# Kernel optimization log

Measured on AMD Instinct MI355X. Metric: run time of the kernel, lower is better.

The kernel has to match this reference:

```python
import jax, jax.numpy as jnp
import numpy as np

HIDDEN = 1024
HEADS = 16
HEAD_DIM = HIDDEN // HEADS

def setup_inputs() -> dict:
    key = jax.random.key(0)
    ks = jax.random.split(key, 11)
    B, T, D = 2, 2048, HIDDEN
    s = 1.0 / np.sqrt(D)
    return {
        "query": jax.random.normal(ks[0], (B, T, D), jnp.float32),
        "key": jax.random.normal(ks[1], (B, T, D), jnp.float32),
        "value": jax.random.normal(ks[2], (B, T, D), jnp.float32),
        "Wq": jax.random.normal(ks[3], (D, D), jnp.float32) * s,
        "bq": jnp.zeros((D,), jnp.float32),
        "Wk": jax.random.normal(ks[4], (D, D), jnp.float32) * s,
        "bk": jnp.zeros((D,), jnp.float32),
        "Wv": jax.random.normal(ks[5], (D, D), jnp.float32) * s,
        "bv": jnp.zeros((D,), jnp.float32),
        "Wo": jax.random.normal(ks[6], (D, D), jnp.float32) * s,
        "bo": jnp.zeros((D,), jnp.float32),
    }

def reference(query, key, value, Wq, bq, Wk, bk, Wv, bv, Wo, bo):
    B, Tq, D = query.shape
    Tk = key.shape[1]
    H, Hd = HEADS, HEAD_DIM
    # projections -> [B, H, T, Hd]
    Q = (query @ Wq + bq).reshape(B, Tq, H, Hd).transpose(0, 2, 1, 3)
    K = (key @ Wk + bk).reshape(B, Tk, H, Hd).transpose(0, 2, 1, 3)
    V = (value @ Wv + bv).reshape(B, Tk, H, Hd).transpose(0, 2, 1, 3)
    scale = jnp.sqrt(jnp.asarray(Hd, Q.dtype))
    scores = jnp.einsum('bhqd,bhkd->bhqk', Q, K) / scale  # [B,H,Tq,Tk]
    causal = jnp.triu(jnp.ones((Tq, Tk), bool), k=1)
    scores = jnp.where(causal[None, None], jnp.asarray(-jnp.inf, scores.dtype), scores)
    attn = jax.nn.softmax(scores, axis=-1)
    out = jnp.einsum('bhqk,bhkd->bhqd', attn, V)  # [B,H,Tq,Hd]
    out = out.transpose(0, 2, 1, 3).reshape(B, Tq, D)
    return out @ Wo + bo
```

## Files before the change

kernel.cpp:

```cpp
#include <hip/hip_runtime.h>
#include <hip/hip_bf16.h>


typedef __bf16 bf16_t;
typedef __bf16 bf16x4 __attribute__((ext_vector_type(4)));
typedef __bf16 bf16x8 __attribute__((ext_vector_type(8)));
typedef float f32x4 __attribute__((ext_vector_type(4)));
typedef float f32x16 __attribute__((ext_vector_type(16)));
typedef unsigned int u32;
typedef unsigned int u32x2v __attribute__((ext_vector_type(2)));
typedef unsigned int u32x4v __attribute__((ext_vector_type(4)));

#define D_MODEL 1024
#define SEQ_T   2048
#define NHEAD   16
#define HDIM    64
#define M_ROWS  4096
#define MEGA    (1024 * 1024)

__device__ __forceinline__ void gl2lds16(const void* g, void* l) {
    __builtin_amdgcn_global_load_lds((const __attribute__((address_space(1))) u32*)g,
                                     (__attribute__((address_space(3))) u32*)l, 16, 0, 0);
}

__device__ __forceinline__ u32 pk2(float a, float b) {
    unsigned short x = __builtin_bit_cast(unsigned short, (bf16_t)a);
    unsigned short y = __builtin_bit_cast(unsigned short, (bf16_t)b);
    return (u32)x | ((u32)y << 16);
}

#define JOB(j, k0, n) ((j) | ((k0) << 8) | ((n) << 16))
__device__ __constant__ int JOBS[47] = {
    JOB(16,0,17),
    JOB(15,0,16), JOB(30,0,16), JOB(31,0,16), JOB(31,16,16),
    JOB(14,0,15), JOB(28,0,15), JOB(29,0,15), JOB(29,15,15), JOB(30,16,15),
    JOB(13,0,14), JOB(26,0,14), JOB(27,0,14), JOB(27,14,14), JOB(28,15,14),
    JOB(12,0,13), JOB(24,0,13), JOB(25,0,13), JOB(25,13,13), JOB(26,14,13),
    JOB(11,0,12), JOB(22,0,12), JOB(23,0,12), JOB(23,12,12), JOB(24,13,12),
    JOB(10,0,11), JOB(20,0,11), JOB(21,0,11), JOB(21,11,11), JOB(22,12,11),
    JOB( 9,0,10), JOB(18,0,10), JOB(19,0,10), JOB(19,10,10), JOB(20,11,10),
    JOB( 8,0, 9), JOB(17,0, 9), JOB(17,9, 9), JOB(18,10, 9),
    JOB( 7,0, 8), JOB( 6,0, 7), JOB( 5,0, 6), JOB( 4,0, 5),
    JOB( 3,0, 4), JOB( 2,0, 3), JOB( 1,0, 2), JOB( 0,0, 1)
};

__global__ __launch_bounds__(256) void prep(
    const float* __restrict__ Wq, const float* __restrict__ Wk,
    const float* __restrict__ Wv, const float* __restrict__ Wo,
    const float* __restrict__ Xq, const float* __restrict__ Xk, const float* __restrict__ Xv,
    bf16_t* __restrict__ Wqt, bf16_t* __restrict__ Wkt,
    bf16_t* __restrict__ Wvt, bf16_t* __restrict__ Wot,
    bf16_t* __restrict__ Xb)
{
    int blk = blockIdx.x, tid = threadIdx.x;
    if (blk < 4096) {
        int wi = blk >> 10, t = blk & 1023;
        int n0 = (t & 31) * 32, k0 = (t >> 5) * 32;
        const float* W = wi == 0 ? Wq : (wi == 1 ? Wk : (wi == 2 ? Wv : Wo));
        bf16_t* Wt = wi == 0 ? Wqt : (wi == 1 ? Wkt : (wi == 2 ? Wvt : Wot));
        __shared__ float tile[32][33];
        int tx = tid & 31, ty = tid >> 5;
#pragma unroll
        for (int i = 0; i < 32; i += 8)
            tile[ty + i][tx] = W[(k0 + ty + i) * D_MODEL + n0 + tx];
        __syncthreads();
#pragma unroll
        for (int i = 0; i < 32; i += 8)
            Wt[(size_t)(n0 + ty + i) * D_MODEL + k0 + tx] = (bf16_t)tile[tx][ty + i];
    } else {
        int b2 = blk - 4096;
        int xi = b2 >> 10;
        const float* X = xi == 0 ? Xq : (xi == 1 ? Xk : Xv);
        bf16_t* XB = Xb + (size_t)xi * M_ROWS * D_MODEL;
        size_t base = (size_t)(b2 & 1023) * 4096 + tid * 16;
        const float4* xp = (const float4*)(X + base);
        float4 a0 = xp[0], a1 = xp[1], a2 = xp[2], a3 = xp[3];
        bf16x8 o0, o1;
        o0[0] = (bf16_t)a0.x; o0[1] = (bf16_t)a0.y; o0[2] = (bf16_t)a0.z; o0[3] = (bf16_t)a0.w;
        o0[4] = (bf16_t)a1.x; o0[5] = (bf16_t)a1.y; o0[6] = (bf16_t)a1.z; o0[7] = (bf16_t)a1.w;
        o1[0] = (bf16_t)a2.x; o1[1] = (bf16_t)a2.y; o1[2] = (bf16_t)a2.z; o1[3] = (bf16_t)a2.w;
        o1[4] = (bf16_t)a3.x; o1[5] = (bf16_t)a3.y; o1[6] = (bf16_t)a3.z; o1[7] = (bf16_t)a3.w;
        *(bf16x8*)(XB + base) = o0;
        *(bf16x8*)(XB + base + 8) = o1;
    }
}

template <bool PRECAST>
__global__ __launch_bounds__(256) void proj_fused(
    const float* __restrict__ Xq, const float* __restrict__ Xk, const float* __restrict__ Xv,
    const bf16_t* __restrict__ Xb,
    const bf16_t* __restrict__ Wqt, const bf16_t* __restrict__ Wkt, const bf16_t* __restrict__ Wvt,
    const float* __restrict__ bq, const float* __restrict__ bk, const float* __restrict__ bv,
    bf16_t* __restrict__ Qh, bf16_t* __restrict__ Kh, bf16_t* __restrict__ Vt)
{
    __shared__ bf16_t Ab[128 * 32];
    __shared__ bf16_t Bb[128 * 32];
    int tid = threadIdx.x;
    int w = tid >> 6, lane = tid & 63, lo16 = lane & 15, quad = lane >> 4;
    int m0 = blockIdx.x * 128;
    int proj = blockIdx.y >> 3;
    int n0 = (blockIdx.y & 7) * 128;
    const float*  X    = proj == 0 ? Xq  : (proj == 1 ? Xk  : Xv);
    const bf16_t* XB   = Xb + (size_t)proj * M_ROWS * D_MODEL;
    const bf16_t* Wt   = proj == 0 ? Wqt : (proj == 1 ? Wkt : Wvt);
    const float*  bias = proj == 0 ? bq  : (proj == 1 ? bk  : bv);
    int wm = (w >> 1) * 64, wn = (w & 1) * 64;

    f32x4 acc[4][4];
#pragma unroll
    for (int i = 0; i < 4; i++)
#pragma unroll
        for (int j = 0; j < 4; j++) acc[i][j] = (f32x4){0.f, 0.f, 0.f, 0.f};

    for (int k0 = 0; k0 < D_MODEL; k0 += 32) {
        __syncthreads();
#pragma unroll
        for (int p = 0; p < 2; p++) {
            int idx = p * 256 + tid;
            int row = idx >> 2, ch = (idx & 3) * 8;
            if (PRECAST) {
                gl2lds16(XB + (size_t)(m0 + row) * D_MODEL + k0 + ch, Ab + idx * 8);
            } else {
                const float* as = X + (size_t)(m0 + row) * D_MODEL + k0 + ch;
                float4 a0 = *(const float4*)as, a1 = *(const float4*)(as + 4);
                bf16x8 av;
                av[0] = (bf16_t)a0.x; av[1] = (bf16_t)a0.y; av[2] = (bf16_t)a0.z; av[3] = (bf16_t)a0.w;
                av[4] = (bf16_t)a1.x; av[5] = (bf16_t)a1.y; av[6] = (bf16_t)a1.z; av[7] = (bf16_t)a1.w;
                *(bf16x8*)(Ab + idx * 8) = av;
            }
            gl2lds16(Wt + (size_t)(n0 + row) * D_MODEL + k0 + ch, Bb + idx * 8);
        }
        __syncthreads();
        bf16x8 af[4], bfr[4];
#pragma unroll
        for (int i = 0; i < 4; i++)
            af[i] = *(bf16x8*)(Ab + (wm + i * 16 + lo16) * 32 + quad * 8);
#pragma unroll
        for (int j = 0; j < 4; j++)
            bfr[j] = *(bf16x8*)(Bb + (wn + j * 16 + lo16) * 32 + quad * 8);
#pragma unroll
        for (int i = 0; i < 4; i++)
#pragma unroll
            for (int j = 0; j < 4; j++)
                acc[i][j] = __builtin_amdgcn_mfma_f32_16x16x32_bf16(af[i], bfr[j], acc[i][j], 0, 0, 0);
    }

    float qscale = proj == 0 ? 0.1803368801111244f : 1.0f;
#pragma unroll
    for (int j = 0; j < 4; j++) {
        int col = n0 + wn + j * 16 + lo16;
        float bv2 = bias[col];
        int h = col >> 6, hd = col & 63;
#pragma unroll
        for (int i = 0; i < 4; i++) {
#pragma unroll
            for (int r = 0; r < 4; r++) {
                int m = m0 + wm + i * 16 + quad * 4 + r;
                int b = m >> 11, t = m & 2047;
                bf16_t val = (bf16_t)((acc[i][j][r] + bv2) * qscale);
                if (proj == 2)
                    Vt[(((size_t)(b * NHEAD + h) * HDIM + hd) * SEQ_T) + t] = val;
                else if (proj == 1)
                    Kh[(((size_t)(b * NHEAD + h) * SEQ_T + t) * HDIM) + hd] = val;
                else
                    Qh[(((size_t)(b * NHEAD + h) * SEQ_T + t) * HDIM) + hd] = val;
            }
        }
    }
}

__global__ __launch_bounds__(128, 2) void flash_attn(const bf16_t* __restrict__ Qh,
                                                     const bf16_t* __restrict__ Kh,
                                                     const bf16_t* __restrict__ Vt,
                                                     bf16_t* __restrict__ Ob,
                                                     float* __restrict__ Pw) {
    int blk = blockIdx.x;
    int bh = blk & 31;
    int enc = JOBS[blk >> 5];
    int j = enc & 255, kt0 = (enc >> 8) & 255, nkt = (enc >> 16) & 255;
    int tid = threadIdx.x;
    int w = tid >> 6, lane = tid & 63;
    int l32 = lane & 31, hi = lane >> 5;
    int qbase = j * 64 + w * 32;

    __shared__ bf16_t KL[2][64 * 64];
    __shared__ bf16_t VL[2][64 * 64];

    const bf16_t* Qp = Qh + (size_t)bh * SEQ_T * HDIM;
    const bf16_t* Kp = Kh + (size_t)bh * SEQ_T * HDIM;
    const bf16_t* Vp = Vt + (size_t)bh * HDIM * SEQ_T;

    bf16x8 qf[4];
    {
        const bf16_t* qr = Qp + (size_t)(qbase + l32) * HDIM;
#pragma unroll
        for (int kd = 0; kd < 4; kd++)
            qf[kd] = *(const bf16x8*)(qr + kd * 16 + hi * 8);
    }

    bf16x8 ones;
#pragma unroll
    for (int i = 0; i < 8; i++) ones[i] = (bf16_t)1.0f;

    f32x16 oacc[2], lacc;
#pragma unroll
    for (int r = 0; r < 16; r++) { oacc[0][r] = 0.f; oacc[1][r] = 0.f; lacc[r] = 0.f; }

#pragma unroll
    for (int p = 0; p < 4; p++) {
        int idx = p * 128 + tid;
        int row = idx >> 3, cp = idx & 7, cl = (cp - row) & 7;
        gl2lds16(Kp + (size_t)(kt0 * 64 + row) * HDIM + cl * 8, KL[0] + idx * 8);
        gl2lds16(Vp + (size_t)row * SEQ_T + kt0 * 64 + cl * 8, VL[0] + idx * 8);
    }

    for (int it = 0; it < nkt; it++) {
        int kt = kt0 + it;
        int cur = it & 1;
        __syncthreads();

        if (it + 1 < nkt) {
#pragma unroll
            for (int p = 0; p < 4; p++) {
                int idx = p * 128 + tid;
                int row = idx >> 3, cp = idx & 7, cl = (cp - row) & 7;
                gl2lds16(Kp + (size_t)((kt + 1) * 64 + row) * HDIM + cl * 8, KL[cur ^ 1] + idx * 8);
                gl2lds16(Vp + (size_t)row * SEQ_T + (kt + 1) * 64 + cl * 8, VL[cur ^ 1] + idx * 8);
            }
        }
        const bf16_t* KLc = KL[cur];
        const bf16_t* VLc = VL[cur];

        f32x16 sacc[2];
#pragma unroll
        for (int r = 0; r < 16; r++) { sacc[0][r] = 0.f; sacc[1][r] = 0.f; }
#pragma unroll
        for (int ks = 0; ks < 2; ks++) {
            int key = l32 + 32 * ks;
#pragma unroll
            for (int kd = 0; kd < 4; kd++) {
                bf16x8 kf = *(const bf16x8*)(KLc + key * 64 + ((2 * kd + hi + key) & 7) * 8);
                sacc[ks] = __builtin_amdgcn_mfma_f32_32x32x16_bf16(kf, qf[kd], sacc[ks], 0, 0, 0);
            }
        }

        bool diag = (kt == j);
        int qg = qbase + l32;
#pragma unroll
        for (int ks = 0; ks < 2; ks++)
#pragma unroll
            for (int r = 0; r < 16; r++) {
                float e = exp2f(sacc[ks][r]);
                if (diag) {
                    int key = kt * 64 + ks * 32 + (r & 3) + 8 * (r >> 2) + 4 * hi;
                    e = (key <= qg) ? e : 0.f;
                }
                sacc[ks][r] = e;
            }

        bf16x8 pf[4];
#pragma unroll
        for (int t = 0; t < 4; t++) {
            const int ks = t >> 1, bb = (t & 1) * 8;
            u32 A1 = pk2(sacc[ks][bb + 0], sacc[ks][bb + 1]);
            u32 A2 = pk2(sacc[ks][bb + 2], sacc[ks][bb + 3]);
            u32 C1 = pk2(sacc[ks][bb + 4], sacc[ks][bb + 5]);
            u32 C2 = pk2(sacc[ks][bb + 6], sacc[ks][bb + 7]);
            u32x2v s1 = __builtin_amdgcn_permlane32_swap(A1, C1, false, false);
            u32x2v s2 = __builtin_amdgcn_permlane32_swap(A2, C2, false, false);
            u32x4v wv; wv[0] = s1[0]; wv[1] = s2[0]; wv[2] = s1[1]; wv[3] = s2[1];
            pf[t] = __builtin_bit_cast(bf16x8, wv);
            lacc = __builtin_amdgcn_mfma_f32_32x32x16_bf16(pf[t], ones, lacc, 0, 0, 0);
        }

#pragma unroll
        for (int dt = 0; dt < 2; dt++) {
            int d = l32 + 32 * dt;
#pragma unroll
            for (int t = 0; t < 4; t++) {
                bf16x8 vf = *(const bf16x8*)(VLc + d * 64 + ((2 * t + hi + d) & 7) * 8);
                oacc[dt] = __builtin_amdgcn_mfma_f32_32x32x16_bf16(pf[t], vf, oacc[dt], 0, 0, 0);
            }
        }
    }

    if (j >= 17) {
        int c = kt0 ? 1 : 0;
        float* slot = Pw + (size_t)((bh * 15 + (j - 17)) * 2 + c) * 4160;
#pragma unroll
        for (int dt = 0; dt < 2; dt++)
#pragma unroll
            for (int r = 0; r < 16; r++) {
                int qrow = w * 32 + (r & 3) + 8 * (r >> 2) + 4 * hi;
                slot[qrow * 64 + l32 + 32 * dt] = oacc[dt][r];
            }
        if (l32 == 0) {
#pragma unroll
            for (int r = 0; r < 16; r++)
                slot[4096 + w * 32 + (r & 3) + 8 * (r >> 2) + 4 * hi] = lacc[r];
        }
    } else {
        int b = bh >> 4, h = bh & 15;
        float inv[16];
#pragma unroll
        for (int r = 0; r < 16; r++) inv[r] = 1.0f / lacc[r];
#pragma unroll
        for (int dt = 0; dt < 2; dt++)
#pragma unroll
            for (int r = 0; r < 16; r++) {
                int q = qbase + (r & 3) + 8 * (r >> 2) + 4 * hi;
                int d = l32 + 32 * dt;
                Ob[((size_t)b * SEQ_T + q) * D_MODEL + h * HDIM + d] = (bf16_t)(oacc[dt][r] * inv[r]);
            }
    }
}

__global__ __launch_bounds__(256) void combine(const float* __restrict__ Pw,
                                               bf16_t* __restrict__ Ob) {
    int blk = blockIdx.x;
    int bh = blk / 15, jj = blk % 15;
    int j = jj + 17;
    int b = bh >> 4, h = bh & 15;
    const float* s0 = Pw + (size_t)blk * 8320;
    const float* s1 = s0 + 4160;
    __shared__ float linv[64];
    int tid = threadIdx.x;
    if (tid < 64) linv[tid] = 1.0f / (s0[4096 + tid] + s1[4096 + tid]);
    __syncthreads();
#pragma unroll
    for (int i = 0; i < 4; i++) {
        int e = i * 1024 + tid * 4;
        f32x4 a = *(const f32x4*)(s0 + e);
        f32x4 c = *(const f32x4*)(s1 + e);
        int q = e >> 6, d = e & 63;
        float il = linv[q];
        bf16x4 o;
        o[0] = (bf16_t)((a[0] + c[0]) * il);
        o[1] = (bf16_t)((a[1] + c[1]) * il);
        o[2] = (bf16_t)((a[2] + c[2]) * il);
        o[3] = (bf16_t)((a[3] + c[3]) * il);
        *(bf16x4*)(Ob + ((size_t)b * SEQ_T + j * 64 + q) * D_MODEL + h * HDIM + d) = o;
    }
}

__global__ __launch_bounds__(256) void out_gemm(const bf16_t* __restrict__ A,
                                                const bf16_t* __restrict__ Wt,
                                                const float* __restrict__ bias,
                                                float* __restrict__ out) {
    __shared__ bf16_t Ab[128 * 32];
    __shared__ bf16_t Bb[128 * 32];
    int tid = threadIdx.x;
    int w = tid >> 6, lane = tid & 63, lo16 = lane & 15, quad = lane >> 4;
    int m0 = blockIdx.x * 128;
    int n0 = blockIdx.y * 128;
    int wm = (w >> 1) * 64, wn = (w & 1) * 64;

    f32x4 acc[4][4];
#pragma unroll
    for (int i = 0; i < 4; i++)
#pragma unroll
        for (int j = 0; j < 4; j++) acc[i][j] = (f32x4){0.f, 0.f, 0.f, 0.f};

    for (int k0 = 0; k0 < D_MODEL; k0 += 32) {
        __syncthreads();
#pragma unroll
        for (int p = 0; p < 2; p++) {
            int idx = p * 256 + tid;
            int row = idx >> 2, ch = (idx & 3) * 8;
            gl2lds16(A  + (size_t)(m0 + row) * D_MODEL + k0 + ch, Ab + idx * 8);
            gl2lds16(Wt + (size_t)(n0 + row) * D_MODEL + k0 + ch, Bb + idx * 8);
        }
        __syncthreads();
        bf16x8 af[4], bfr[4];
#pragma unroll
        for (int i = 0; i < 4; i++)
            af[i] = *(bf16x8*)(Ab + (wm + i * 16 + lo16) * 32 + quad * 8);
#pragma unroll
        for (int j = 0; j < 4; j++)
            bfr[j] = *(bf16x8*)(Bb + (wn + j * 16 + lo16) * 32 + quad * 8);
#pragma unroll
        for (int i = 0; i < 4; i++)
#pragma unroll
            for (int j = 0; j < 4; j++)
                acc[i][j] = __builtin_amdgcn_mfma_f32_16x16x32_bf16(af[i], bfr[j], acc[i][j], 0, 0, 0);
    }

#pragma unroll
    for (int j = 0; j < 4; j++) {
        int col = n0 + wn + j * 16 + lo16;
        float bv2 = bias[col];
#pragma unroll
        for (int i = 0; i < 4; i++)
#pragma unroll
            for (int r = 0; r < 4; r++) {
                int m = m0 + wm + i * 16 + quad * 4 + r;
                out[(size_t)m * D_MODEL + col] = acc[i][j][r] + bv2;
            }
    }
}

extern "C" void kernel_launch(void* const* d_in, const int* in_sizes, int n_in,
                              void* d_out, int out_size, void* d_ws, size_t ws_size,
                              hipStream_t stream) {
    const float* q  = (const float*)d_in[0];
    const float* k  = (const float*)d_in[1];
    const float* v  = (const float*)d_in[2];
    const float* Wq = (const float*)d_in[3];
    const float* bq = (const float*)d_in[4];
    const float* Wk = (const float*)d_in[5];
    const float* bk = (const float*)d_in[6];
    const float* Wv = (const float*)d_in[7];
    const float* bv = (const float*)d_in[8];
    const float* Wo = (const float*)d_in[9];
    const float* bo = (const float*)d_in[10];
    float* out = (float*)d_out;

    bf16_t* Wqt = (bf16_t*)d_ws;
    bf16_t* Wkt = Wqt + (size_t)MEGA;
    bf16_t* Wvt = Wkt + (size_t)MEGA;
    bf16_t* Wot = Wvt + (size_t)MEGA;
    bf16_t* Qh  = Wot + (size_t)MEGA;
    bf16_t* Kh  = Qh  + (size_t)M_ROWS * D_MODEL;
    bf16_t* Vt  = Kh  + (size_t)M_ROWS * D_MODEL;
    bf16_t* Xb  = Vt  + (size_t)M_ROWS * D_MODEL;
    bf16_t* Ob  = Xb;
    float*  Pw  = (float*)(Xb + (size_t)M_ROWS * D_MODEL);

    bool precast = ws_size >= (size_t)(4 * MEGA + 3 * M_ROWS * D_MODEL + 3 * M_ROWS * D_MODEL) * sizeof(bf16_t);

    int prep_blocks = precast ? 4096 + 3 * 1024 : 4096;
    prep<<<prep_blocks, 256, 0, stream>>>(Wq, Wk, Wv, Wo, q, k, v, Wqt, Wkt, Wvt, Wot, Xb);

    dim3 pg(M_ROWS / 128, 24);
    if (precast)
        proj_fused<true><<<pg, 256, 0, stream>>>(q, k, v, Xb, Wqt, Wkt, Wvt, bq, bk, bv, Qh, Kh, Vt);
    else
        proj_fused<false><<<pg, 256, 0, stream>>>(q, k, v, Xb, Wqt, Wkt, Wvt, bq, bk, bv, Qh, Kh, Vt);

    flash_attn<<<47 * 32, 128, 0, stream>>>(Qh, Kh, Vt, Ob, Pw);
    combine<<<32 * 15, 256, 0, stream>>>(Pw, Ob);

    dim3 og(M_ROWS / 128, D_MODEL / 128);
    out_gemm<<<og, 256, 0, stream>>>(Ob, Wot, bo, out);
}
```

Before: 238.1 us.

## Use 128-query flash-attention blocks with rebalanced split-K job table and n-way combine

Each flash-attention workgroup now covers 128 queries with four waves instead of 64 with two, so every K/V tile staged in LDS is shared by twice as many queries. A new 34-entry job table splits long causal rows into chunks of up to 10 key tiles to balance work. Partial results go to per-bh slots, which may spill into the output buffer when the workspace is small, and a generalized combine kernel sums 2 to 4 partials. Waves whose diagonal comes earlier skip tiles past it, and s_setprio is raised around the MFMA sections. In exchange there are more partial writes and reads, plus some idle waves on the diagonal tiles.

New measurement: 235.0 us. About the same (-1.3%).

```diff
diff --git a/kernel.cpp b/kernel.cpp
--- a/kernel.cpp
+++ b/kernel.cpp
@@ -29,20 +29,42 @@
     return (u32)x | ((u32)y << 16);
 }
 
-#define JOB(j, k0, n) ((j) | ((k0) << 8) | ((n) << 16))
-__device__ __constant__ int JOBS[47] = {
-    JOB(16,0,17),
-    JOB(15,0,16), JOB(30,0,16), JOB(31,0,16), JOB(31,16,16),
-    JOB(14,0,15), JOB(28,0,15), JOB(29,0,15), JOB(29,15,15), JOB(30,16,15),
-    JOB(13,0,14), JOB(26,0,14), JOB(27,0,14), JOB(27,14,14), JOB(28,15,14),
-    JOB(12,0,13), JOB(24,0,13), JOB(25,0,13), JOB(25,13,13), JOB(26,14,13),
-    JOB(11,0,12), JOB(22,0,12), JOB(23,0,12), JOB(23,12,12), JOB(24,13,12),
-    JOB(10,0,11), JOB(20,0,11), JOB(21,0,11), JOB(21,11,11), JOB(22,12,11),
-    JOB( 9,0,10), JOB(18,0,10), JOB(19,0,10), JOB(19,10,10), JOB(20,11,10),
-    JOB( 8,0, 9), JOB(17,0, 9), JOB(17,9, 9), JOB(18,10, 9),
-    JOB( 7,0, 8), JOB( 6,0, 7), JOB( 5,0, 6), JOB( 4,0, 5),
-    JOB( 3,0, 4), JOB( 2,0, 3), JOB( 1,0, 2), JOB( 0,0, 1)
+#define JOB4(j, k0, n, s, m) ((j) | ((k0) << 4) | ((n) << 10) | ((s) << 14) | ((m) << 19))
+__device__ __constant__ int JOBS4[34] = {
+    JOB4(4, 0, 10, 0, 0),
+    JOB4(9, 0, 10, 8, 1),  JOB4(9, 10, 10, 9, 1),
+    JOB4(13, 0, 10, 19, 1),
+    JOB4(14, 0, 10, 22, 1), JOB4(14, 10, 10, 23, 1), JOB4(14, 20, 10, 24, 1),
+    JOB4(8, 0, 9, 6, 1),   JOB4(8, 9, 9, 7, 1),
+    JOB4(12, 0, 9, 16, 1), JOB4(12, 9, 9, 17, 1),
+    JOB4(13, 10, 9, 20, 1), JOB4(13, 19, 9, 21, 1),
+    JOB4(3, 0, 8, 0, 0),
+    JOB4(7, 0, 8, 4, 1),   JOB4(7, 8, 8, 5, 1),
+    JOB4(10, 0, 8, 10, 1),
+    JOB4(11, 0, 8, 13, 1), JOB4(11, 8, 8, 14, 1), JOB4(11, 16, 8, 15, 1),
+    JOB4(12, 18, 8, 18, 1),
+    JOB4(15, 0, 8, 25, 1), JOB4(15, 8, 8, 26, 1), JOB4(15, 16, 8, 27, 1), JOB4(15, 24, 8, 28, 1),
+    JOB4(6, 0, 7, 2, 1),   JOB4(6, 7, 7, 3, 1),
+    JOB4(10, 8, 7, 11, 1), JOB4(10, 15, 7, 12, 1),
+    JOB4(2, 0, 6, 0, 0),
+    JOB4(5, 0, 6, 0, 1),   JOB4(5, 6, 6, 1, 1),
+    JOB4(1, 0, 4, 0, 0),
+    JOB4(0, 0, 2, 0, 0)
 };
+__device__ __constant__ int CMB4[11] = {
+    5 | (2 << 4) | (0 << 8),  6 | (2 << 4) | (2 << 8),  7 | (2 << 4) | (4 << 8),
+    8 | (2 << 4) | (6 << 8),  9 | (2 << 4) | (8 << 8),  10 | (3 << 4) | (10 << 8),
+    11 | (3 << 4) | (13 << 8), 12 | (3 << 4) | (16 << 8), 13 | (3 << 4) | (19 << 8),
+    14 | (3 << 4) | (22 << 8), 15 | (4 << 4) | (25 << 8)
+};
+#define SLOTS_PER_BH 29
+#define SLOT_F       8320
+#define SLOTS_IN_A   504
+
+__device__ __forceinline__ float* slot_ptr(float* PwA, float* PwB, int s) {
+    return s < SLOTS_IN_A ? PwA + (size_t)s * SLOT_F
+                          : PwB + (size_t)(s - SLOTS_IN_A) * SLOT_F;
+}
 
 __global__ __launch_bounds__(256) void prep(
     const float* __restrict__ Wq, const float* __restrict__ Wk,
@@ -169,19 +191,22 @@
     }
 }
 
-__global__ __launch_bounds__(128, 2) void flash_attn(const bf16_t* __restrict__ Qh,
+__global__ __launch_bounds__(256, 2) void flash_attn(const bf16_t* __restrict__ Qh,
                                                      const bf16_t* __restrict__ Kh,
                                                      const bf16_t* __restrict__ Vt,
                                                      bf16_t* __restrict__ Ob,
-                                                     float* __restrict__ Pw) {
+                                                     float* __restrict__ PwA,
+                                                     float* __restrict__ PwB) {
     int blk = blockIdx.x;
     int bh = blk & 31;
-    int enc = JOBS[blk >> 5];
-    int j = enc & 255, kt0 = (enc >> 8) & 255, nkt = (enc >> 16) & 255;
+    int enc = JOBS4[blk >> 5];
+    int j4 = enc & 15, kt0 = (enc >> 4) & 63, nkt = (enc >> 10) & 15;
+    int slot = (enc >> 14) & 31, multi = (enc >> 19) & 1;
     int tid = threadIdx.x;
     int w = tid >> 6, lane = tid & 63;
     int l32 = lane & 31, hi = lane >> 5;
-    int qbase = j * 64 + w * 32;
+    int qbase = j4 * 128 + w * 32;
+    int diagkt = 2 * j4 + (w >> 1);
 
     __shared__ bf16_t KL[2][64 * 64];
     __shared__ bf16_t VL[2][64 * 64];
@@ -207,8 +232,8 @@
     for (int r = 0; r < 16; r++) { oacc[0][r] = 0.f; oacc[1][r] = 0.f; lacc[r] = 0.f; }
 
 #pragma unroll
-    for (int p = 0; p < 4; p++) {
-        int idx = p * 128 + tid;
+    for (int p = 0; p < 2; p++) {
+        int idx = p * 256 + tid;
         int row = idx >> 3, cp = idx & 7, cl = (cp - row) & 7;
         gl2lds16(Kp + (size_t)(kt0 * 64 + row) * HDIM + cl * 8, KL[0] + idx * 8);
         gl2lds16(Vp + (size_t)row * SEQ_T + kt0 * 64 + cl * 8, VL[0] + idx * 8);
@@ -221,19 +246,21 @@
 
         if (it + 1 < nkt) {
 #pragma unroll
-            for (int p = 0; p < 4; p++) {
-                int idx = p * 128 + tid;
+            for (int p = 0; p < 2; p++) {
+                int idx = p * 256 + tid;
                 int row = idx >> 3, cp = idx & 7, cl = (cp - row) & 7;
                 gl2lds16(Kp + (size_t)((kt + 1) * 64 + row) * HDIM + cl * 8, KL[cur ^ 1] + idx * 8);
                 gl2lds16(Vp + (size_t)row * SEQ_T + (kt + 1) * 64 + cl * 8, VL[cur ^ 1] + idx * 8);
             }
         }
+        if (kt > diagkt) continue;
         const bf16_t* KLc = KL[cur];
         const bf16_t* VLc = VL[cur];
 
         f32x16 sacc[2];
 #pragma unroll
         for (int r = 0; r < 16; r++) { sacc[0][r] = 0.f; sacc[1][r] = 0.f; }
+        __builtin_amdgcn_s_setprio(1);
 #pragma unroll
         for (int ks = 0; ks < 2; ks++) {
             int key = l32 + 32 * ks;
@@ -243,8 +270,9 @@
                 sacc[ks] = __builtin_amdgcn_mfma_f32_32x32x16_bf16(kf, qf[kd], sacc[ks], 0, 0, 0);
             }
         }
-
-        bool diag = (kt == j);
+        __builtin_amdgcn_s_setprio(0);
+
+        bool diag = (kt == diagkt);
         int qg = qbase + l32;
 #pragma unroll
         for (int ks = 0; ks < 2; ks++)
@@ -273,6 +301,7 @@
             lacc = __builtin_amdgcn_mfma_f32_32x32x16_bf16(pf[t], ones, lacc, 0, 0, 0);
         }
 
+        __builtin_amdgcn_s_setprio(1);
 #pragma unroll
         for (int dt = 0; dt < 2; dt++) {
             int d = l32 + 32 * dt;
@@ -282,22 +311,22 @@
                 oacc[dt] = __builtin_amdgcn_mfma_f32_32x32x16_bf16(pf[t], vf, oacc[dt], 0, 0, 0);
             }
         }
-    }
-
-    if (j >= 17) {
-        int c = kt0 ? 1 : 0;
-        float* slot = Pw + (size_t)((bh * 15 + (j - 17)) * 2 + c) * 4160;
+        __builtin_amdgcn_s_setprio(0);
+    }
+
+    if (multi) {
+        float* sp = slot_ptr(PwA, PwB, bh * SLOTS_PER_BH + slot);
 #pragma unroll
         for (int dt = 0; dt < 2; dt++)
 #pragma unroll
             for (int r = 0; r < 16; r++) {
                 int qrow = w * 32 + (r & 3) + 8 * (r >> 2) + 4 * hi;
-                slot[qrow * 64 + l32 + 32 * dt] = oacc[dt][r];
+                sp[qrow * 64 + l32 + 32 * dt] = oacc[dt][r];
             }
         if (l32 == 0) {
 #pragma unroll
             for (int r = 0; r < 16; r++)
-                slot[4096 + w * 32 + (r & 3) + 8 * (r >> 2) + 4 * hi] = lacc[r];
+                sp[8192 + w * 32 + (r & 3) + 8 * (r >> 2) + 4 * hi] = lacc[r];
         }
     } else {
         int b = bh >> 4, h = bh & 15;
@@ -315,31 +344,37 @@
     }
 }
 
-__global__ __launch_bounds__(256) void combine(const float* __restrict__ Pw,
+__global__ __launch_bounds__(256) void combine(float* __restrict__ PwA,
+                                               float* __restrict__ PwB,
                                                bf16_t* __restrict__ Ob) {
     int blk = blockIdx.x;
-    int bh = blk / 15, jj = blk % 15;
-    int j = jj + 17;
+    int bh = blk / 11, e = blk % 11;
+    int info = CMB4[e];
+    int j4 = info & 15, c = (info >> 4) & 7, base = info >> 8;
+    int s0 = bh * SLOTS_PER_BH + base;
     int b = bh >> 4, h = bh & 15;
-    const float* s0 = Pw + (size_t)blk * 8320;
-    const float* s1 = s0 + 4160;
-    __shared__ float linv[64];
     int tid = threadIdx.x;
-    if (tid < 64) linv[tid] = 1.0f / (s0[4096 + tid] + s1[4096 + tid]);
+    __shared__ float linv[128];
+    if (tid < 128) {
+        float s = 0.f;
+        for (int k = 0; k < c; k++) s += slot_ptr(PwA, PwB, s0 + k)[8192 + tid];
+        linv[tid] = 1.0f / s;
+    }
     __syncthreads();
 #pragma unroll
-    for (int i = 0; i < 4; i++) {
-        int e = i * 1024 + tid * 4;
-        f32x4 a = *(const f32x4*)(s0 + e);
-        f32x4 c = *(const f32x4*)(s1 + e);
-        int q = e >> 6, d = e & 63;
+    for (int i = 0; i < 8; i++) {
+        int e4 = i * 1024 + tid * 4;
+        f32x4 a = (f32x4){0.f, 0.f, 0.f, 0.f};
+        for (int k = 0; k < c; k++) {
+            f32x4 v = *(const f32x4*)(slot_ptr(PwA, PwB, s0 + k) + e4);
+            a[0] += v[0]; a[1] += v[1]; a[2] += v[2]; a[3] += v[3];
+        }
+        int q = e4 >> 6, d = e4 & 63;
         float il = linv[q];
         bf16x4 o;
-        o[0] = (bf16_t)((a[0] + c[0]) * il);
-        o[1] = (bf16_t)((a[1] + c[1]) * il);
-        o[2] = (bf16_t)((a[2] + c[2]) * il);
-        o[3] = (bf16_t)((a[3] + c[3]) * il);
-        *(bf16x4*)(Ob + ((size_t)b * SEQ_T + j * 64 + q) * D_MODEL + h * HDIM + d) = o;
+        o[0] = (bf16_t)(a[0] * il); o[1] = (bf16_t)(a[1] * il);
+        o[2] = (bf16_t)(a[2] * il); o[3] = (bf16_t)(a[3] * il);
+        *(bf16x4*)(Ob + ((size_t)b * SEQ_T + j4 * 128 + q) * D_MODEL + h * HDIM + d) = o;
     }
 }
 
@@ -424,9 +459,14 @@
     bf16_t* Vt  = Kh  + (size_t)M_ROWS * D_MODEL;
     bf16_t* Xb  = Vt  + (size_t)M_ROWS * D_MODEL;
     bf16_t* Ob  = Xb;
-    float*  Pw  = (float*)(Xb + (size_t)M_ROWS * D_MODEL);
-
-    bool precast = ws_size >= (size_t)(4 * MEGA + 3 * M_ROWS * D_MODEL + 3 * M_ROWS * D_MODEL) * sizeof(bf16_t);
+    float*  PwA = (float*)(Xb + (size_t)M_ROWS * D_MODEL);
+    bf16_t* ws_end = Xb + (size_t)3 * M_ROWS * D_MODEL;
+
+    size_t used_bytes = (size_t)(4 * MEGA + 6 * M_ROWS * D_MODEL) * sizeof(bf16_t);
+    size_t pwb_bytes  = (size_t)(928 - SLOTS_IN_A) * SLOT_F * sizeof(float);
+    float* PwB = (ws_size >= used_bytes + pwb_bytes) ? (float*)ws_end : (float*)d_out;
+
+    bool precast = ws_size >= used_bytes;
 
     int prep_blocks = precast ? 4096 + 3 * 1024 : 4096;
     prep<<<prep_blocks, 256, 0, stream>>>(Wq, Wk, Wv, Wo, q, k, v, Wqt, Wkt, Wvt, Wot, Xb);
@@ -437,8 +477,8 @@
     else
         proj_fused<false><<<pg, 256, 0, stream>>>(q, k, v, Xb, Wqt, Wkt, Wvt, bq, bk, bv, Qh, Kh, Vt);
 
-    flash_attn<<<47 * 32, 128, 0, stream>>>(Qh, Kh, Vt, Ob, Pw);
-    combine<<<32 * 15, 256, 0, stream>>>(Pw, Ob);
+    flash_attn<<<34 * 32, 256, 0, stream>>>(Qh, Kh, Vt, Ob, PwA, PwB);
+    combine<<<11 * 32, 256, 0, stream>>>(PwA, PwB, Ob);
 
     dim3 og(M_ROWS / 128, D_MODEL / 128);
     out_gemm<<<og, 256, 0, stream>>>(Ob, Wot, bo, out);
```
